# Optimization experiments

Hardware: AMD Instinct MI355X
Metric: run time of the kernel (lower is better)

Reference implementation:

```python
import jax, jax.numpy as jnp
import numpy as np

N = 100000          # num nodes
E = 3200000         # num edges (avg degree 32)
G = 64              # num graphs in batch
F_IN = 2            # num_node_features
H = 16              # hidden_size
NUM_LAYERS = 2


def sage_conv(x, src, dst, W_l, b_l, W_r):
    # PyG SAGEConv (mean aggr): out = lin_l(mean_{j in N(i)} x_j) + lin_r(x_i)
    msg = x[src]                                                  # [E, F] gather
    agg = jax.ops.segment_sum(msg, dst, num_segments=N)          # [N, F] scatter-add
    deg = jax.ops.segment_sum(jnp.ones((src.shape[0],), x.dtype), dst, num_segments=N)
    mean = agg / jnp.maximum(deg, 1.0)[:, None]
    return mean @ W_l + b_l + x @ W_r


def setup_inputs() -> dict:
    key = jax.random.key(0)
    ks = jax.random.split(key, 10)
    x = jax.random.normal(ks[0], (N, F_IN), dtype=jnp.float32)
    edge_index = jax.random.randint(ks[1], (2, E), 0, N, dtype=jnp.int64)
    batch = jnp.sort(jax.random.randint(ks[2], (N,), 0, G, dtype=jnp.int64))
    s1 = 1.0 / np.sqrt(F_IN)
    s2 = 1.0 / np.sqrt(H)
    return {
        "x": x,
        "edge_index": edge_index,
        "batch": batch,
        "W1_l": jax.random.uniform(ks[3], (F_IN, H), jnp.float32, -s1, s1),
        "b1_l": jnp.zeros((H,), jnp.float32),
        "W1_r": jax.random.uniform(ks[4], (F_IN, H), jnp.float32, -s1, s1),
        "W2_l": jax.random.uniform(ks[5], (H, H), jnp.float32, -s2, s2),
        "b2_l": jnp.zeros((H,), jnp.float32),
        "W2_r": jax.random.uniform(ks[6], (H, H), jnp.float32, -s2, s2),
        "W_end": jax.random.uniform(ks[7], (H, 1), jnp.float32, -s2, s2),
        "b_end": jnp.zeros((1,), jnp.float32),
    }


def reference(x, edge_index, batch, W1_l, b1_l, W1_r, W2_l, b2_l, W2_r, W_end, b_end):
    src, dst = edge_index[0], edge_index[1]
    h = sage_conv(x, src, dst, W1_l, b1_l, W1_r)                 # conv1
    for _ in range(NUM_LAYERS - 1):
        h = jax.nn.relu(h)
        h = sage_conv(h, src, dst, W2_l, b2_l, W2_r)             # conv2
    h = jax.nn.relu(h)
    # dropout is identity in eval mode
    h = h @ W_end + b_end                                         # [N, 1]
    # global mean pool over graphs
    summed = jax.ops.segment_sum(h, batch, num_segments=G)       # [G, 1]
    counts = jax.ops.segment_sum(jnp.ones((N,), h.dtype), batch, num_segments=G)
    pooled = summed / jnp.maximum(counts, 1.0)[:, None]
    return jax.nn.sigmoid(pooled)                                 # [G, 1]
```

## Files before the change

### kernel.cpp

```cpp
#include <hip/hip_runtime.h>
#include <math.h>

#define NN 100000
#define NE 3200000
#define NG 64
#define HID 16
#define EPB 4096
#define NBLKE ((NE + EPB - 1) / EPB)
#define NBUCK ((NN + 255) / 256)
#define LMAX 10240

typedef unsigned int uint;
typedef float vf2 __attribute__((ext_vector_type(2)));


template <bool HI>
__device__ inline vf2 dec2fp8(uint u) {
#if __has_builtin(__builtin_amdgcn_cvt_pk_f32_fp8)
    return __builtin_amdgcn_cvt_pk_f32_fp8((int)u, HI);
#else
    vf2 r;
    uint b0 = (u >> (HI ? 16 : 0)) & 0xff;
    uint b1 = (u >> (HI ? 24 : 8)) & 0xff;
    uint em0 = b0 & 0x7f, em1 = b1 & 0x7f;
    float v0 = (em0 >= 8) ? __uint_as_float(((em0 >> 3) + 120) << 23 | (em0 & 7) << 20)
                          : (float)em0 * 0.001953125f;
    float v1 = (em1 >= 8) ? __uint_as_float(((em1 >> 3) + 120) << 23 | (em1 & 7) << 20)
                          : (float)em1 * 0.001953125f;
    r.x = (b0 & 0x80) ? -v0 : v0;
    r.y = (b1 & 0x80) ? -v1 : v1;
    return r;
#endif
}

__device__ inline uint enc1fp8(float f) {
    if (!(f > 0.f)) return 0u;
    f = fminf(f, 448.f);
    uint b = __float_as_uint(f);
    int e = (int)(b >> 23) - 127;
    if (e >= -6) {
        uint m = b & 0x7fffffu;
        uint r = (m + 0x7ffffu + ((m >> 20) & 1u)) >> 20;
        uint code = ((uint)(e + 7) << 3) + r;
        return code > 126u ? 126u : code;
    }
    float t = f * 512.f;
    return (uint)(t + 0.5f);
}

template <bool HI>
__device__ inline uint packfp8x2(float a, float b, uint old) {
#if __has_builtin(__builtin_amdgcn_cvt_pk_fp8_f32)
    return (uint)__builtin_amdgcn_cvt_pk_fp8_f32(a, b, (int)old, HI);
#else
    uint v = enc1fp8(a) | (enc1fp8(b) << 8);
    return HI ? ((old & 0x0000ffffu) | (v << 16)) : ((old & 0xffff0000u) | v);
#endif
}

__global__ __launch_bounds__(512) void k_bhist(const int* __restrict__ dst,
                                               int* __restrict__ blockCnt) {
    __shared__ int h[NBUCK];
    int t = threadIdx.x;
    for (int i = t; i < NBUCK; i += 512) h[i] = 0;
    __syncthreads();
    int base = blockIdx.x * EPB;
    int n4 = (min(base + EPB, NE) - base) >> 2;
    const int4* d4 = (const int4*)(dst + base);
    for (int i = t; i < n4; i += 512) {
        int4 v = d4[i];
        atomicAdd(&h[v.x >> 8], 1);
        atomicAdd(&h[v.y >> 8], 1);
        atomicAdd(&h[v.z >> 8], 1);
        atomicAdd(&h[v.w >> 8], 1);
    }
    __syncthreads();
    for (int i = t; i < NBUCK; i += 512)
        blockCnt[i * NBLKE + blockIdx.x] = h[i];
}

__global__ __launch_bounds__(1024) void k_bucketscan(int* __restrict__ blockCnt,
                                                     int* __restrict__ bucketTot) {
    __shared__ int a[1024];
    int t = threadIdx.x, b = blockIdx.x;
    a[t] = (t < NBLKE) ? blockCnt[b * NBLKE + t] : 0;
    __syncthreads();
    for (int off = 1; off < 1024; off <<= 1) {
        int x = a[t] + ((t >= off) ? a[t - off] : 0);
        __syncthreads();
        a[t] = x;
        __syncthreads();
    }
    if (t < NBLKE) blockCnt[b * NBLKE + t] = (t ? a[t - 1] : 0);
    if (t == 0) bucketTot[b] = a[1023];
}

__global__ __launch_bounds__(512) void k_basescan(const int* __restrict__ bucketTot,
                                                  int* __restrict__ bucketBase,
                                                  int* __restrict__ offs,
                                                  float* __restrict__ gsum,
                                                  float* __restrict__ gcnt) {
    __shared__ int a[512];
    int t = threadIdx.x;
    if (t < NG) { gsum[t] = 0.f; gcnt[t] = 0.f; }
    a[t] = (t < NBUCK) ? bucketTot[t] : 0;
    __syncthreads();
    for (int off = 1; off < 512; off <<= 1) {
        int x = a[t] + ((t >= off) ? a[t - off] : 0);
        __syncthreads();
        a[t] = x;
        __syncthreads();
    }
    if (t < NBUCK) bucketBase[t] = (t ? a[t - 1] : 0);
    if (t == 0) { bucketBase[NBUCK] = a[511]; offs[NN] = a[511]; }
}

__global__ __launch_bounds__(512) void k_bscatter(const int* __restrict__ src,
                                                  const int* __restrict__ dst,
                                                  const int* __restrict__ blockCnt,
                                                  const int* __restrict__ bucketBase,
                                                  int* __restrict__ pairs) {
    __shared__ int cur[NBUCK];
    int t = threadIdx.x;
    for (int i = t; i < NBUCK; i += 512)
        cur[i] = blockCnt[i * NBLKE + blockIdx.x] + bucketBase[i];
    __syncthreads();
    int base = blockIdx.x * EPB;
    int n4 = (min(base + EPB, NE) - base) >> 2;
    const int4* d4 = (const int4*)(dst + base);
    const int4* s4 = (const int4*)(src + base);
    for (int i = t; i < n4; i += 512) {
        int4 dv = d4[i];
        int4 sv = s4[i];
        int p0 = atomicAdd(&cur[dv.x >> 8], 1);
        pairs[p0] = (sv.x << 8) | (dv.x & 255);
        int p1 = atomicAdd(&cur[dv.y >> 8], 1);
        pairs[p1] = (sv.y << 8) | (dv.y & 255);
        int p2 = atomicAdd(&cur[dv.z >> 8], 1);
        pairs[p2] = (sv.z << 8) | (dv.z & 255);
        int p3 = atomicAdd(&cur[dv.w >> 8], 1);
        pairs[p3] = (sv.w << 8) | (dv.w & 255);
    }
}

__global__ __launch_bounds__(512) void k_fill2c1(
    const int* __restrict__ bucketBase, const int* __restrict__ pairs,
    const float* __restrict__ x,
    const float* __restrict__ W1l, const float* __restrict__ b1l,
    const float* __restrict__ W1r,
    int* __restrict__ offs, int* __restrict__ csr, uint* __restrict__ h8) {
    __shared__ int a[256];
    __shared__ int lcur[256];
    __shared__ int lss[LMAX];
    int t = threadIdx.x, b = blockIdx.x;
    int pb = bucketBase[b], pe = bucketBase[b + 1];
    if (t < 256) a[t] = 0;
    __syncthreads();
    for (int e = pb + t; e < pe; e += 512)
        atomicAdd(&a[pairs[e] & 255], 1);
    __syncthreads();
    for (int off = 1; off < 256; off <<= 1) {
        int v = 0;
        if (t < 256) v = a[t] + ((t >= off) ? a[t - off] : 0);
        __syncthreads();
        if (t < 256) a[t] = v;
        __syncthreads();
    }
    if (t < 256) lcur[t] = t ? a[t - 1] : 0;
    __syncthreads();
    for (int e = pb + t; e < pe; e += 512) {
        int v = pairs[e];
        int s = v >> 8, dl = v & 255;
        int lpos = atomicAdd(&lcur[dl], 1);
        csr[pb + lpos] = s;
        if (lpos < LMAX) lss[lpos] = s;
    }
    __syncthreads();
    if (t < 256) {
        int node = b * 256 + t;
        if (node < NN) {
            int excl = t ? a[t - 1] : 0;
            int cntn = a[t] - excl;
            offs[node] = pb + excl;
            float s0 = 0.f, s1 = 0.f;
            for (int k = 0; k < cntn; ++k) {
                int idx = excl + k;
                int s = (idx < LMAX) ? lss[idx] : csr[pb + idx];
                float2 xv = *(const float2*)(x + 2 * s);
                s0 += xv.x; s1 += xv.y;
            }
            float inv = 1.0f / fmaxf((float)cntn, 1.0f);
            float m0 = s0 * inv, m1 = s1 * inv;
            float x0 = x[2 * node], x1 = x[2 * node + 1];
            float o[16];
#pragma unroll
            for (int h = 0; h < 16; ++h)
                o[h] = fmaxf(m0 * W1l[h] + m1 * W1l[16 + h] + b1l[h]
                           + x0 * W1r[h] + x1 * W1r[16 + h], 0.f);
            uint4 w;
            w.x = packfp8x2<false>(o[0],  o[1],  0u);
            w.x = packfp8x2<true >(o[2],  o[3],  w.x);
            w.y = packfp8x2<false>(o[4],  o[5],  0u);
            w.y = packfp8x2<true >(o[6],  o[7],  w.y);
            w.z = packfp8x2<false>(o[8],  o[9],  0u);
            w.z = packfp8x2<true >(o[10], o[11], w.z);
            w.w = packfp8x2<false>(o[12], o[13], 0u);
            w.w = packfp8x2<true >(o[14], o[15], w.w);
            *(uint4*)(h8 + (size_t)node * 4) = w;
        }
    }
}

__global__ __launch_bounds__(256) void k_conv2pool(
    const int* __restrict__ offs, const int* __restrict__ csr,
    const uint* __restrict__ h8,
    const float* __restrict__ W2l, const float* __restrict__ b2l,
    const float* __restrict__ W2r, const float* __restrict__ Wend,
    const float* __restrict__ bend, const int* __restrict__ batch,
    float* __restrict__ gsum, float* __restrict__ gcnt) {
    __shared__ float sWl[256], sWr[256], sB[HID], sWe[HID];
    __shared__ float sm[64][17], shr[64][17];
    __shared__ float ls[NG], lc[NG];
    int t = threadIdx.x;
    sWl[t] = W2l[t];
    sWr[t] = W2r[t];
    if (t < HID) { sB[t] = b2l[t]; sWe[t] = Wend[t]; }
    if (t < NG) { ls[t] = 0.f; lc[t] = 0.f; }

    int g = t >> 2;
    int l4 = t & 3;
    int gbase = (t & 63) & 60;
    int i = blockIdx.x * 64 + g;
    int beg = 0, end = 0;
    if (i < NN) { beg = offs[i]; end = offs[i + 1]; }
    float a0 = 0.f, a1 = 0.f, a2 = 0.f, a3 = 0.f;
    int kb = beg;
    uint ub[8];
    for (; kb + 8 <= end; kb += 8) {
        int sv0 = csr[kb + l4];
        int sv1 = csr[kb + 4 + l4];
#pragma unroll
        for (int j = 0; j < 4; ++j) {
            int s = __shfl(sv0, gbase + j, 64);
            ub[j] = h8[(size_t)s * 4 + l4];
        }
#pragma unroll
        for (int j = 0; j < 4; ++j) {
            int s = __shfl(sv1, gbase + j, 64);
            ub[4 + j] = h8[(size_t)s * 4 + l4];
        }
#pragma unroll
        for (int j = 0; j < 8; ++j) {
            vf2 p0 = dec2fp8<false>(ub[j]);
            vf2 p1 = dec2fp8<true >(ub[j]);
            a0 += p0.x; a1 += p0.y; a2 += p1.x; a3 += p1.y;
        }
    }
    for (; kb + 4 <= end; kb += 4) {
        int sv = csr[kb + l4];
#pragma unroll
        for (int j = 0; j < 4; ++j) {
            int s = __shfl(sv, gbase + j, 64);
            ub[j] = h8[(size_t)s * 4 + l4];
        }
#pragma unroll
        for (int j = 0; j < 4; ++j) {
            vf2 p0 = dec2fp8<false>(ub[j]);
            vf2 p1 = dec2fp8<true >(ub[j]);
            a0 += p0.x; a1 += p0.y; a2 += p1.x; a3 += p1.y;
        }
    }
    if (kb < end) {
        int idx = kb + l4;
        int sv = (idx < end) ? csr[idx] : 0;
        int nb = end - kb;
        for (int j = 0; j < nb; ++j) {
            int s = __shfl(sv, gbase + j, 64);
            uint u = h8[(size_t)s * 4 + l4];
            vf2 p0 = dec2fp8<false>(u);
            vf2 p1 = dec2fp8<true >(u);
            a0 += p0.x; a1 += p0.y; a2 += p1.x; a3 += p1.y;
        }
    }
    if (i < NN) {
        float inv = 1.0f / fmaxf((float)(end - beg), 1.0f);
        uint us = h8[(size_t)i * 4 + l4];
        vf2 q0 = dec2fp8<false>(us);
        vf2 q1 = dec2fp8<true >(us);
        sm[g][4 * l4 + 0] = a0 * inv;
        sm[g][4 * l4 + 1] = a1 * inv;
        sm[g][4 * l4 + 2] = a2 * inv;
        sm[g][4 * l4 + 3] = a3 * inv;
        shr[g][4 * l4 + 0] = q0.x;
        shr[g][4 * l4 + 1] = q0.y;
        shr[g][4 * l4 + 2] = q1.x;
        shr[g][4 * l4 + 3] = q1.y;
    }
    __syncthreads();

    float y = 0.f;
    if (i < NN) {
#pragma unroll
        for (int k = 0; k < 4; ++k) {
            int h = 4 * l4 + k;
            float a = sB[h];
#pragma unroll
            for (int f = 0; f < HID; ++f)
                a += sm[g][f] * sWl[f * HID + h] + shr[g][f] * sWr[f * HID + h];
            y += fmaxf(a, 0.f) * sWe[h];
        }
    }
    y += __shfl_xor(y, 1, 64);
    y += __shfl_xor(y, 2, 64);
    if (l4 == 0 && i < NN) {
        int bg = batch[i];
        atomicAdd(&ls[bg], y + bend[0]);
        atomicAdd(&lc[bg], 1.0f);
    }
    __syncthreads();
    if (t < NG && lc[t] != 0.0f) {
        unsafeAtomicAdd(&gsum[t], ls[t]);
        unsafeAtomicAdd(&gcnt[t], lc[t]);
    }
}

__global__ void k_final(const float* __restrict__ gsum, const float* __restrict__ gcnt,
                        float* __restrict__ out) {
    int g = threadIdx.x;
    if (g < NG) {
        float p = gsum[g] / fmaxf(gcnt[g], 1.0f);
        out[g] = 1.0f / (1.0f + expf(-p));
    }
}

extern "C" void kernel_launch(void* const* d_in, const int* in_sizes, int n_in,
                              void* d_out, int out_size, void* d_ws, size_t ws_size,
                              hipStream_t stream) {
    const float* x    = (const float*)d_in[0];
    const int*   ei   = (const int*)d_in[1];
    const int*   batch= (const int*)d_in[2];
    const float* W1l  = (const float*)d_in[3];
    const float* b1l  = (const float*)d_in[4];
    const float* W1r  = (const float*)d_in[5];
    const float* W2l  = (const float*)d_in[6];
    const float* b2l  = (const float*)d_in[7];
    const float* W2r  = (const float*)d_in[8];
    const float* Wend = (const float*)d_in[9];
    const float* bend = (const float*)d_in[10];

    const int* src = ei;
    const int* dst = ei + NE;

    float* gsum      = (float*)d_ws;
    float* gcnt      = (float*)d_ws + NG;
    int*   blockCnt  = (int*)d_ws + 2 * NG;
    int*   bucketTot = blockCnt + (size_t)NBUCK * NBLKE;
    int*   bucketBase= bucketTot + NBUCK;
    int*   offs      = bucketBase + NBUCK + 1;
    size_t po        = (size_t)(offs - (int*)d_ws) + NN + 1;
    po               = (po + 3) & ~(size_t)3;
    int*   pairs     = (int*)d_ws + po;
    int*   csr       = pairs + NE;
    uint*  h8        = (uint*)(csr + NE);

    k_bhist     <<<NBLKE, 512, 0, stream>>>(dst, blockCnt);
    k_bucketscan<<<NBUCK, 1024, 0, stream>>>(blockCnt, bucketTot);
    k_basescan  <<<1, 512, 0, stream>>>(bucketTot, bucketBase, offs, gsum, gcnt);
    k_bscatter  <<<NBLKE, 512, 0, stream>>>(src, dst, blockCnt, bucketBase, pairs);
    k_fill2c1   <<<NBUCK, 512, 0, stream>>>(bucketBase, pairs, x, W1l, b1l, W1r,
                                            offs, csr, h8);
    k_conv2pool <<<(NN + 63) / 64, 256, 0, stream>>>(offs, csr, h8, W2l, b2l, W2r,
                                                     Wend, bend, batch, gsum, gcnt);
    k_final     <<<1, 64, 0, stream>>>(gsum, gcnt, (float*)d_out);
}
```

Measured before the change: 109.7 us.

## Merge bucket scans into one kernel and parallelize conv1 aggregation

Bucket totals are now built by global atomics inside the histogram kernel, so the per-bucket scan and the base scan run as one launch with an extra block. This removes one kernel launch and its serialization, at the cost of an added memset. In the fill kernel, the local histogram is split across two wave-parity copies to reduce LDS atomic contention. The CSR is written coalesced from shared memory instead of by scattered writes. The conv1 neighbor sum now uses all 512 threads, two per node, instead of 256, combining the halves through shared memory.

```diff
diff --git a/kernel.cpp b/kernel.cpp
--- a/kernel.cpp
+++ b/kernel.cpp
@@ -59,7 +59,8 @@
 }
 
 __global__ __launch_bounds__(512) void k_bhist(const int* __restrict__ dst,
-                                               int* __restrict__ blockCnt) {
+                                               int* __restrict__ blockCnt,
+                                               int* __restrict__ bucketTot) {
     __shared__ int h[NBUCK];
     int t = threadIdx.x;
     for (int i = t; i < NBUCK; i += 512) h[i] = 0;
@@ -75,44 +76,44 @@
         atomicAdd(&h[v.w >> 8], 1);
     }
     __syncthreads();
-    for (int i = t; i < NBUCK; i += 512)
-        blockCnt[i * NBLKE + blockIdx.x] = h[i];
-}
-
-__global__ __launch_bounds__(1024) void k_bucketscan(int* __restrict__ blockCnt,
-                                                     int* __restrict__ bucketTot) {
+    for (int i = t; i < NBUCK; i += 512) {
+        int hv = h[i];
+        blockCnt[i * NBLKE + blockIdx.x] = hv;
+        if (hv) atomicAdd(&bucketTot[i], hv);
+    }
+}
+
+__global__ __launch_bounds__(1024) void k_scan(int* __restrict__ blockCnt,
+                                               const int* __restrict__ bucketTot,
+                                               int* __restrict__ bucketBase,
+                                               int* __restrict__ offs,
+                                               float* __restrict__ gsum,
+                                               float* __restrict__ gcnt) {
     __shared__ int a[1024];
     int t = threadIdx.x, b = blockIdx.x;
-    a[t] = (t < NBLKE) ? blockCnt[b * NBLKE + t] : 0;
-    __syncthreads();
-    for (int off = 1; off < 1024; off <<= 1) {
-        int x = a[t] + ((t >= off) ? a[t - off] : 0);
+    if (b < NBUCK) {
+        a[t] = (t < NBLKE) ? blockCnt[b * NBLKE + t] : 0;
         __syncthreads();
-        a[t] = x;
+        for (int off = 1; off < 1024; off <<= 1) {
+            int x = a[t] + ((t >= off) ? a[t - off] : 0);
+            __syncthreads();
+            a[t] = x;
+            __syncthreads();
+        }
+        if (t < NBLKE) blockCnt[b * NBLKE + t] = (t ? a[t - 1] : 0);
+    } else {
+        if (t < NG) { gsum[t] = 0.f; gcnt[t] = 0.f; }
+        a[t] = (t < NBUCK) ? bucketTot[t] : 0;
         __syncthreads();
-    }
-    if (t < NBLKE) blockCnt[b * NBLKE + t] = (t ? a[t - 1] : 0);
-    if (t == 0) bucketTot[b] = a[1023];
-}
-
-__global__ __launch_bounds__(512) void k_basescan(const int* __restrict__ bucketTot,
-                                                  int* __restrict__ bucketBase,
-                                                  int* __restrict__ offs,
-                                                  float* __restrict__ gsum,
-                                                  float* __restrict__ gcnt) {
-    __shared__ int a[512];
-    int t = threadIdx.x;
-    if (t < NG) { gsum[t] = 0.f; gcnt[t] = 0.f; }
-    a[t] = (t < NBUCK) ? bucketTot[t] : 0;
-    __syncthreads();
-    for (int off = 1; off < 512; off <<= 1) {
-        int x = a[t] + ((t >= off) ? a[t - off] : 0);
-        __syncthreads();
-        a[t] = x;
-        __syncthreads();
-    }
-    if (t < NBUCK) bucketBase[t] = (t ? a[t - 1] : 0);
-    if (t == 0) { bucketBase[NBUCK] = a[511]; offs[NN] = a[511]; }
+        for (int off = 1; off < 1024; off <<= 1) {
+            int x = a[t] + ((t >= off) ? a[t - off] : 0);
+            __syncthreads();
+            a[t] = x;
+            __syncthreads();
+        }
+        if (t < NBUCK) bucketBase[t] = (t ? a[t - 1] : 0);
+        if (t == 0) { bucketBase[NBUCK] = a[1023]; offs[NN] = a[1023]; }
+    }
 }
 
 __global__ __launch_bounds__(512) void k_bscatter(const int* __restrict__ src,
@@ -149,15 +150,20 @@
     const float* __restrict__ W1l, const float* __restrict__ b1l,
     const float* __restrict__ W1r,
     int* __restrict__ offs, int* __restrict__ csr, uint* __restrict__ h8) {
+    __shared__ int aH[2][256];
     __shared__ int a[256];
     __shared__ int lcur[256];
     __shared__ int lss[LMAX];
+    __shared__ float ps0[512], ps1[512];
     int t = threadIdx.x, b = blockIdx.x;
     int pb = bucketBase[b], pe = bucketBase[b + 1];
-    if (t < 256) a[t] = 0;
-    __syncthreads();
+    if (t < 256) { aH[0][t] = 0; aH[1][t] = 0; }
+    __syncthreads();
+    int wp = (t >> 6) & 1;
     for (int e = pb + t; e < pe; e += 512)
-        atomicAdd(&a[pairs[e] & 255], 1);
+        atomicAdd(&aH[wp][pairs[e] & 255], 1);
+    __syncthreads();
+    if (t < 256) a[t] = aH[0][t] + aH[1][t];
     __syncthreads();
     for (int off = 1; off < 256; off <<= 1) {
         int v = 0;
@@ -172,8 +178,27 @@
         int v = pairs[e];
         int s = v >> 8, dl = v & 255;
         int lpos = atomicAdd(&lcur[dl], 1);
-        csr[pb + lpos] = s;
         if (lpos < LMAX) lss[lpos] = s;
+        else csr[pb + lpos] = s;
+    }
+    __syncthreads();
+    int tot = pe - pb;
+    int totL = min(tot, LMAX);
+    for (int idx = t; idx < totL; idx += 512)
+        csr[pb + idx] = lss[idx];
+    {
+        int node8 = t & 255;
+        int half = t >> 8;
+        int excl = node8 ? a[node8 - 1] : 0;
+        int cntn = a[node8] - excl;
+        float s0 = 0.f, s1 = 0.f;
+        for (int k = half; k < cntn; k += 2) {
+            int idx = excl + k;
+            int s = (idx < LMAX) ? lss[idx] : csr[pb + idx];
+            float2 xv = *(const float2*)(x + 2 * s);
+            s0 += xv.x; s1 += xv.y;
+        }
+        ps0[t] = s0; ps1[t] = s1;
     }
     __syncthreads();
     if (t < 256) {
@@ -182,15 +207,9 @@
             int excl = t ? a[t - 1] : 0;
             int cntn = a[t] - excl;
             offs[node] = pb + excl;
-            float s0 = 0.f, s1 = 0.f;
-            for (int k = 0; k < cntn; ++k) {
-                int idx = excl + k;
-                int s = (idx < LMAX) ? lss[idx] : csr[pb + idx];
-                float2 xv = *(const float2*)(x + 2 * s);
-                s0 += xv.x; s1 += xv.y;
-            }
             float inv = 1.0f / fmaxf((float)cntn, 1.0f);
-            float m0 = s0 * inv, m1 = s1 * inv;
+            float m0 = (ps0[t] + ps0[t + 256]) * inv;
+            float m1 = (ps1[t] + ps1[t + 256]) * inv;
             float x0 = x[2 * node], x1 = x[2 * node + 1];
             float o[16];
 #pragma unroll
@@ -363,9 +382,10 @@
     int*   csr       = pairs + NE;
     uint*  h8        = (uint*)(csr + NE);
 
-    k_bhist     <<<NBLKE, 512, 0, stream>>>(dst, blockCnt);
-    k_bucketscan<<<NBUCK, 1024, 0, stream>>>(blockCnt, bucketTot);
-    k_basescan  <<<1, 512, 0, stream>>>(bucketTot, bucketBase, offs, gsum, gcnt);
+    hipMemsetAsync(bucketTot, 0, NBUCK * sizeof(int), stream);
+    k_bhist     <<<NBLKE, 512, 0, stream>>>(dst, blockCnt, bucketTot);
+    k_scan      <<<NBUCK + 1, 1024, 0, stream>>>(blockCnt, bucketTot, bucketBase,
+                                                 offs, gsum, gcnt);
     k_bscatter  <<<NBLKE, 512, 0, stream>>>(src, dst, blockCnt, bucketBase, pairs);
     k_fill2c1   <<<NBUCK, 512, 0, stream>>>(bucketBase, pairs, x, W1l, b1l, W1r,
                                             offs, csr, h8);
```

Measured after the change: 126.9 us. 1.16x slower.
